# Optimization experiments

Hardware: AMD Instinct MI355X
Metric: run time of the kernel (lower is better)

## Reference

```python
import jax, jax.numpy as jnp
import numpy as np
from jax import lax

NPOINT = 1024
NSAMPLES = (16, 32, 64)
BN_EPS = 1e-5


def fps(xyz, npoint):
    """Farthest point sampling. xyz: [B,N,3] -> idx [B,npoint].
    Deterministic start at index 0 (torch version uses a random start)."""
    B, N, _ = xyz.shape

    def step(carry, _):
        dist, far = carry
        centroid = jnp.take_along_axis(xyz, far[:, None, None], axis=1)  # [B,1,3]
        d = jnp.sum((xyz - centroid) ** 2, axis=-1)                      # [B,N]
        dist = jnp.minimum(dist, d)
        nxt = jnp.argmax(dist, axis=1)
        return (dist, nxt), far

    init = (jnp.full((B, N), 1e10, xyz.dtype), jnp.zeros((B,), jnp.int32))
    _, idxs = lax.scan(step, init, None, length=npoint)  # [npoint,B]
    return idxs.T


def gather_points(points, idx):
    # points [B,N,C], idx [B,...] -> [B,...,C]
    return jax.vmap(lambda p, i: p[i])(points, idx)


def sq_cdist(a, b):
    # a [B,S,3], b [B,N,3] -> squared distances [B,S,N] (same ordering as cdist)
    aa = jnp.sum(a * a, -1)[:, :, None]
    bb = jnp.sum(b * b, -1)[:, None, :]
    return aa + bb - 2.0 * jnp.einsum('bsc,bnc->bsn', a, b)


def mlp_scale(g, ws, gs, bs):
    # g: [B,S,k,Cin]; 1x1 conv + BatchNorm (training-mode stats) + ReLU per layer
    for w, gm, bt in zip(ws, gs, bs):
        g = jnp.einsum('bskc,oc->bsko', g, w)
        mu = jnp.mean(g, axis=(0, 1, 2))
        var = jnp.var(g, axis=(0, 1, 2))
        g = jax.nn.relu((g - mu) * lax.rsqrt(var + BN_EPS) * gm + bt)
    return g


def setup_inputs() -> dict:
    key = jax.random.key(0)
    ks = jax.random.split(key, 16)
    B, N, C = 16, 4096, 64
    xyz = jax.random.normal(ks[0], (B, N, 3), jnp.float32)
    features = jax.random.normal(ks[1], (B, N, C), jnp.float32)
    # stacked per-scale MLP params; layer dims: 67 -> 64 -> 64 -> 128
    w0 = jax.random.normal(ks[2], (3, 64, 67), jnp.float32) * 0.1
    w1 = jax.random.normal(ks[3], (3, 64, 64), jnp.float32) * 0.1
    w2 = jax.random.normal(ks[4], (3, 128, 64), jnp.float32) * 0.1
    g0 = jnp.ones((3, 64), jnp.float32); b0 = jnp.zeros((3, 64), jnp.float32)
    g1 = jnp.ones((3, 64), jnp.float32); b1 = jnp.zeros((3, 64), jnp.float32)
    g2 = jnp.ones((3, 128), jnp.float32); b2 = jnp.zeros((3, 128), jnp.float32)
    return {"xyz": xyz, "features": features, "w0": w0, "w1": w1, "w2": w2,
            "g0": g0, "g1": g1, "g2": g2, "b0": b0, "b1": b1, "b2": b2}


def reference(xyz, features, w0, w1, w2, g0, g1, g2, b0, b1, b2):
    fps_idx = fps(xyz, NPOINT)                                   # [B,S]
    new_xyz = jnp.take_along_axis(xyz, fps_idx[..., None], axis=1)  # [B,S,3]
    d2 = sq_cdist(new_xyz, xyz)                                  # [B,S,N]
    outs = []
    for s, nsample in enumerate(NSAMPLES):
        _, idx = lax.top_k(-d2, nsample)                         # k nearest, [B,S,k]
        grouped_xyz = gather_points(xyz, idx) - new_xyz[:, :, None, :]
        grouped_f = gather_points(features, idx)
        g = jnp.concatenate([grouped_xyz, grouped_f], axis=-1)   # [B,S,k,67]
        g = mlp_scale(g, (w0[s], w1[s], w2[s]), (g0[s], g1[s], g2[s]), (b0[s], b1[s], b2[s]))
        outs.append(jnp.max(g, axis=2))                          # max over neighbors -> [B,S,128]
    fused = jnp.concatenate(outs, axis=-1)                       # [B,S,384]
    return new_xyz, fused
```

## Files before the change

### kernel.cpp

```cpp
#include <hip/hip_runtime.h>
#include <stdint.h>

#define BATCH 16
#define NPTS  4096
#define NSAMP 1024

typedef __attribute__((ext_vector_type(8))) short  short8;
typedef __attribute__((ext_vector_type(4))) float  floatx4;

__device__ __forceinline__ unsigned short f2bf(float f) {
    unsigned u = __float_as_uint(f);
    unsigned r = (u + 0x7FFFu + ((u >> 16) & 1u)) >> 16;
    return (unsigned short)r;
}

template<int CTRL>
__device__ __forceinline__ uint64_t dpp_max_u64(uint64_t k) {
    int lo = (int)(unsigned)k;
    int hi = (int)(unsigned)(k >> 32);
    int lo2 = __builtin_amdgcn_update_dpp(0, lo, CTRL, 0xF, 0xF, false);
    int hi2 = __builtin_amdgcn_update_dpp(0, hi, CTRL, 0xF, 0xF, false);
    uint64_t o = ((uint64_t)(unsigned)hi2 << 32) | (unsigned)lo2;
    return o > k ? o : k;
}

#define WT_S 18432

__global__ __launch_bounds__(512) void fps_conv_kernel(
    const float* __restrict__ xyz,
    float* __restrict__ out_xyz,
    const float* __restrict__ feat,
    unsigned short* __restrict__ featb,
    int staged,
    const float* __restrict__ w0, const float* __restrict__ w1,
    const float* __restrict__ w2, unsigned short* __restrict__ wtab)
{
#pragma clang fp contract(off)
    const int wbase = 16 + (staged ? 1024 : 0);
    if (blockIdx.x >= (unsigned)wbase) {
        int t = (blockIdx.x - wbase) * 512 + threadIdx.x;
        if (t < 3*WT_S) {
            int s = t / WT_S, r = t % WT_S;
            unsigned short v = 0;
            if (r < 6144) {
                int n = r / 96, kg = r % 96;
                if (kg < 67) {
                    int ci = (kg < 64) ? (kg + 3) : (kg - 64);
                    v = f2bf(w0[(size_t)(s*64 + n)*67 + ci]);
                }
            } else if (r < 10240) {
                int idx = r - 6144;
                v = f2bf(w1[(size_t)(s*64 + (idx >> 6))*64 + (idx & 63)]);
            } else {
                int idx = r - 10240;
                v = f2bf(w2[(size_t)(s*128 + (idx >> 6))*64 + (idx & 63)]);
            }
            wtab[t] = v;
        }
        return;
    }
    if (blockIdx.x >= 16) {
        int t = (blockIdx.x - 16) * 512 + threadIdx.x;
        const float4* fp = (const float4*)feat + (size_t)t*2;
        float4 a = fp[0], c = fp[1];
        uint4 o;
        o.x = (unsigned)f2bf(a.x) | ((unsigned)f2bf(a.y) << 16);
        o.y = (unsigned)f2bf(a.z) | ((unsigned)f2bf(a.w) << 16);
        o.z = (unsigned)f2bf(c.x) | ((unsigned)f2bf(c.y) << 16);
        o.w = (unsigned)f2bf(c.z) | ((unsigned)f2bf(c.w) << 16);
        ((uint4*)featb)[t] = o;
        return;
    }

    const int b    = blockIdx.x;
    const int tid  = threadIdx.x;
    const int lane = tid & 63;
    const int wave = tid >> 6;
    const float* xb = xyz + (size_t)b * NPTS * 3;

    __shared__ float xsh[NPTS], ysh[NPTS], zsh[NPTS];
    __shared__ float cents[NSAMP * 3];
    __shared__ uint64_t keylds[2][8];

    float px[8], py[8], pz[8], dist[8];
#pragma unroll
    for (int i = 0; i < 8; ++i) {
        int p = tid + (i << 9);
        px[i] = xb[p*3+0];
        py[i] = xb[p*3+1];
        pz[i] = xb[p*3+2];
        dist[i] = 1e10f;
        xsh[p] = px[i]; ysh[p] = py[i]; zsh[p] = pz[i];
    }
    __syncthreads();

    float cx = xb[0], cy = xb[1], cz = xb[2];

    for (int it = 0; it < NSAMP; ++it) {
        if (tid == 0) {
            cents[it*3+0] = cx; cents[it*3+1] = cy; cents[it*3+2] = cz;
        }
        if (it == NSAMP - 1) break;

#pragma unroll
        for (int i = 0; i < 8; ++i) {
            float dx = px[i] - cx, dy = py[i] - cy, dz = pz[i] - cz;
            float d = dx*dx; d = d + dy*dy; d = d + dz*dz;
            dist[i] = fminf(dist[i], d);
        }
        float w01 = dist[1] > dist[0] ? dist[1] : dist[0];
        int   e01 = dist[1] > dist[0] ? 1 : 0;
        float w23 = dist[3] > dist[2] ? dist[3] : dist[2];
        int   e23 = dist[3] > dist[2] ? 3 : 2;
        float w45 = dist[5] > dist[4] ? dist[5] : dist[4];
        int   e45 = dist[5] > dist[4] ? 5 : 4;
        float w67 = dist[7] > dist[6] ? dist[7] : dist[6];
        int   e67 = dist[7] > dist[6] ? 7 : 6;
        float wa  = w23 > w01 ? w23 : w01;
        int   ea  = w23 > w01 ? e23 : e01;
        float wb  = w67 > w45 ? w67 : w45;
        int   eb  = w67 > w45 ? e67 : e45;
        float wv  = wb > wa ? wb : wa;
        int   wi  = wb > wa ? eb : ea;
        unsigned widx = (unsigned)(tid + (wi << 9));
        uint64_t kk = ((uint64_t)__float_as_uint(wv) << 32) | (~widx);

        kk = dpp_max_u64<0x121>(kk);
        kk = dpp_max_u64<0x122>(kk);
        kk = dpp_max_u64<0x124>(kk);
        kk = dpp_max_u64<0x128>(kk);
        kk = dpp_max_u64<0x142>(kk);
        kk = dpp_max_u64<0x143>(kk);

        int pb = it & 1;
        if (lane == 63) keylds[pb][wave] = kk;
        __syncthreads();

        uint64_t f = keylds[pb][lane & 7];
        f = dpp_max_u64<0x121>(f);
        f = dpp_max_u64<0x122>(f);
        f = dpp_max_u64<0x124>(f);
        int cur = (int)~((unsigned)f);

        cx = xsh[cur]; cy = ysh[cur]; cz = zsh[cur];
    }

    __syncthreads();
    for (int i = tid; i < NSAMP*3; i += 512)
        out_xyz[(size_t)b*NSAMP*3 + i] = cents[i];
}

__global__ __launch_bounds__(1024) void knn_kernel(
    const float* __restrict__ xyz,
    const float* __restrict__ new_xyz,
    unsigned short* __restrict__ knn_idx)
{
#pragma clang fp contract(off)
    __shared__ float xs[NPTS], ys[NPTS], zs[NPTS];
    __shared__ uint64_t buf[16][64];
    const int tid  = threadIdx.x;
    const int lane = tid & 63;
    const int wave = tid >> 6;
    const int q = blockIdx.x * 16 + wave;
    const int b = q >> 10;
    const float* xb = xyz + (size_t)b * NPTS * 3;

    for (int i = tid; i < NPTS; i += 1024) {
        xs[i] = xb[i*3+0];
        ys[i] = xb[i*3+1];
        zs[i] = xb[i*3+2];
    }
    __syncthreads();

    const float qx = new_xyz[q*3+0], qy = new_xyz[q*3+1], qz = new_xyz[q*3+2];
    float aa = qx*qx; aa = aa + qy*qy; aa = aa + qz*qz;

    auto keyof = [&](int c) -> unsigned {
        float x = xs[c], y = ys[c], z = zs[c];
        float bb = x*x;  bb = bb + y*y;   bb = bb + z*z;
        float dt = qx*x; dt = dt + qy*y;  dt = dt + qz*z;
        float d2 = (aa + bb) - 2.0f*dt;
        unsigned u = __float_as_uint(d2);
        return (u & 0x80000000u) ? ~u : (u | 0x80000000u);
    };
    auto shfl64 = [&](uint64_t v, int src) -> uint64_t {
        int lo = __shfl((int)(unsigned)v, src);
        int hi = __shfl((int)(unsigned)(v >> 32), src);
        return ((uint64_t)(unsigned)hi << 32) | (unsigned)lo;
    };
    auto shflx64 = [&](uint64_t v, int m) -> uint64_t {
        int lo = __shfl_xor((int)(unsigned)v, m);
        int hi = __shfl_xor((int)(unsigned)(v >> 32), m);
        return ((uint64_t)(unsigned)hi << 32) | (unsigned)lo;
    };
    auto sortP = [&](uint64_t &p) {
#pragma unroll
        for (int kk = 2; kk <= 64; kk <<= 1) {
#pragma unroll
            for (int j = kk >> 1; j >= 1; j >>= 1) {
                uint64_t o = shflx64(p, j);
                bool up    = ((lane & kk) == 0);
                bool lower = ((lane & j) == 0);
                bool oless = o < p;
                bool keep  = (up == lower) ? oless : !oless;
                if (keep) p = o;
            }
        }
    };
    auto mergeP = [&](uint64_t &P, uint64_t Bv) {
        uint64_t rev = shfl64(Bv, 63 - lane);
        if (rev < P) P = rev;
#pragma unroll
        for (int j = 32; j >= 1; j >>= 1) {
            uint64_t o = shflx64(P, j);
            bool lower = ((lane & j) == 0);
            bool oless = o < P;
            bool keep  = lower ? oless : !oless;
            if (keep) P = o;
        }
    };

    uint64_t P = ((uint64_t)keyof(lane) << 32) | (unsigned)lane;
    sortP(P);
    uint64_t Pmax = shfl64(P, 63);
    int cnt = 0;

    for (int bt = 1; bt < 64; ++bt) {
        int c = (bt << 6) + lane;
        uint64_t cand = ((uint64_t)keyof(c) << 32) | (unsigned)c;
        bool qual = cand < Pmax;
        unsigned long long mask = __ballot(qual);
        if (mask == 0ull) continue;
        int n = __popcll(mask);
        if (cnt + n > 64) {
            uint64_t Bv = (lane < cnt) ? buf[wave][lane] : ~0ull;
            sortP(Bv);
            mergeP(P, Bv);
            Pmax = shfl64(P, 63);
            cnt = 0;
            qual = qual && (cand < Pmax);
            mask = __ballot(qual);
            n = __popcll(mask);
        }
        if (qual) {
            int pos = cnt + __popcll(mask & ((1ull << lane) - 1ull));
            buf[wave][pos] = cand;
        }
        cnt += n;
    }
    if (cnt > 0) {
        uint64_t Bv = (lane < cnt) ? buf[wave][lane] : ~0ull;
        sortP(Bv);
        mergeP(P, Bv);
    }
    knn_idx[(size_t)q*64 + lane] = (unsigned short)(P & 0xFFFFu);
}

#define GPB 8

template<int PHASE>
__global__ __launch_bounds__(256) void mlp_phase(
    const float* __restrict__ xyz,
    const float* __restrict__ feat,
    const float* __restrict__ new_xyz,
    const unsigned short* __restrict__ knn,
    const unsigned short* __restrict__ featb,
    int staged,
    const unsigned short* __restrict__ wtab,
    const float* __restrict__ bnp,
    float* __restrict__ stats,
    float* __restrict__ out1)
{
    __shared__ __align__(16) unsigned short g_lds[64*104];
    __shared__ __align__(16) unsigned short a_lds[64*72];
    __shared__ float stat_lds[256];
    __shared__ float wavemax[4*128];

    const int tid  = threadIdx.x;
    const int lane = tid & 63;
    const int wave = tid >> 6;
    const int n16  = lane & 15;
    const int quad = lane >> 4;

    int scale, g0;
    {
        int xcd = blockIdx.x & 7;
        int r   = blockIdx.x >> 3;
        int hi  = (r >= 224) ? 1 : 0;
        int bt  = 2*xcd + hi;
        int r2  = r - hi*224;
        if (r2 < 32)       { scale = 0; g0 = bt*256  + r2*GPB; }
        else if (r2 < 96)  { scale = 1; g0 = bt*512  + (r2-32)*GPB; }
        else               { scale = 2; g0 = bt*1024 + (r2-96)*GPB; }
    }
    const int KNB = 16 << scale;
    const int cpg = 4 >> scale;
    const int wpc = 1 << scale;

    const unsigned short* wt  = wtab + scale * WT_S;
    const unsigned short* w2b = wt + 6144;
    const unsigned short* w3b = wt + 10240;

    short8 w1f[4][3];
#pragma unroll
    for (int nt = 0; nt < 4; ++nt)
#pragma unroll
        for (int kb = 0; kb < 3; ++kb)
            w1f[nt][kb] = *(const short8*)&wt[(nt*16 + n16)*96 + kb*32 + quad*8];

    float s1p[4], t1p[4], s2p[4], t2p[4];
    if constexpr (PHASE >= 2) {
#pragma unroll
        for (int nt = 0; nt < 4; ++nt) {
            int o = ((0*3 + scale)*128 + nt*16 + n16)*2;
            s1p[nt] = bnp[o]; t1p[nt] = bnp[o+1];
        }
    }
    if constexpr (PHASE >= 3) {
#pragma unroll
        for (int nt = 0; nt < 4; ++nt) {
            int o = ((1*3 + scale)*128 + nt*16 + n16)*2;
            s2p[nt] = bnp[o]; t2p[nt] = bnp[o+1];
        }
    }

    float sac[8], sqac[8];
#pragma unroll
    for (int i = 0; i < 8; ++i) { sac[i] = 0.f; sqac[i] = 0.f; }
    stat_lds[tid] = 0.f;
    {
        const int r = tid >> 2;
        const int sub = tid & 3;
        if (sub == 0)      *(uint4*)&g_lds[r*104 + 72] = make_uint4(0u,0u,0u,0u);
        else if (sub == 1) *(uint4*)&g_lds[r*104 + 80] = make_uint4(0u,0u,0u,0u);
        else if (sub == 2) *(uint4*)&g_lds[r*104 + 88] = make_uint4(0u,0u,0u,0u);
    }
    __syncthreads();

    for (int g = g0; g < g0 + GPB; ++g) {
        const int cb = g * cpg;
        {
            const int r   = tid >> 2;
            const int sub = tid & 3;
            const int ci  = cb + (r >> (4 + scale));
            const int j   = r & (KNB - 1);
            const int n   = knn[(size_t)ci*64 + j];
            const int b   = ci >> 10;
            if (staged) {
                const unsigned short* frow = featb + ((size_t)(b*NPTS + n))*64 + sub*16;
                uint4 c0 = ((const uint4*)frow)[0];
                uint4 c1 = ((const uint4*)frow)[1];
                *(uint4*)&g_lds[r*104 + sub*16]     = c0;
                *(uint4*)&g_lds[r*104 + sub*16 + 8] = c1;
            } else {
                const float* frow = feat + ((size_t)(b*NPTS + n))*64 + sub*16;
                unsigned short h[16];
#pragma unroll
                for (int u = 0; u < 16; ++u) h[u] = f2bf(frow[u]);
                uint4 p0, p1;
                p0.x = (unsigned)h[0]  | ((unsigned)h[1]  << 16);
                p0.y = (unsigned)h[2]  | ((unsigned)h[3]  << 16);
                p0.z = (unsigned)h[4]  | ((unsigned)h[5]  << 16);
                p0.w = (unsigned)h[6]  | ((unsigned)h[7]  << 16);
                p1.x = (unsigned)h[8]  | ((unsigned)h[9]  << 16);
                p1.y = (unsigned)h[10] | ((unsigned)h[11] << 16);
                p1.z = (unsigned)h[12] | ((unsigned)h[13] << 16);
                p1.w = (unsigned)h[14] | ((unsigned)h[15] << 16);
                *(uint4*)&g_lds[r*104 + sub*16]     = p0;
                *(uint4*)&g_lds[r*104 + sub*16 + 8] = p1;
            }
            if (sub == 0) {
                const float* nx = new_xyz + (size_t)ci*3;
                const float* xp = xyz + ((size_t)(b*NPTS + n))*3;
                unsigned short h0 = f2bf(xp[0] - nx[0]);
                unsigned short h1 = f2bf(xp[1] - nx[1]);
                unsigned short h2 = f2bf(xp[2] - nx[2]);
                uint4 z = make_uint4((unsigned)h0 | ((unsigned)h1 << 16),
                                     (unsigned)h2, 0u, 0u);
                *(uint4*)&g_lds[r*104 + 64] = z;
            }
        }
        __syncthreads();

        const int rb = wave*16 + n16;
        short8 a0 = *(const short8*)&g_lds[rb*104 +      quad*8];
        short8 a1 = *(const short8*)&g_lds[rb*104 + 32 + quad*8];
        short8 a2 = *(const short8*)&g_lds[rb*104 + 64 + quad*8];
        floatx4 acc[4];
#pragma unroll
        for (int nt = 0; nt < 4; ++nt) {
            floatx4 c = {0.f,0.f,0.f,0.f};
            c = __builtin_amdgcn_mfma_f32_16x16x32_bf16(a0, w1f[nt][0], c, 0,0,0);
            c = __builtin_amdgcn_mfma_f32_16x16x32_bf16(a1, w1f[nt][1], c, 0,0,0);
            c = __builtin_amdgcn_mfma_f32_16x16x32_bf16(a2, w1f[nt][2], c, 0,0,0);
            acc[nt] = c;
        }

        if constexpr (PHASE == 1) {
#pragma unroll
            for (int nt = 0; nt < 4; ++nt) {
                floatx4 c = acc[nt];
                sac[nt]  += c[0]+c[1]+c[2]+c[3];
                sqac[nt] += c[0]*c[0]+c[1]*c[1]+c[2]*c[2]+c[3]*c[3];
            }
        }
        if constexpr (PHASE >= 2) {
#pragma unroll
            for (int nt = 0; nt < 4; ++nt) {
                int ch = nt*16 + n16;
#pragma unroll
                for (int r = 0; r < 4; ++r) {
                    float v = acc[nt][r]*s1p[nt] + t1p[nt];
                    v = fmaxf(v, 0.f);
                    a_lds[(wave*16 + quad*4 + r)*72 + ch] = f2bf(v);
                }
            }
            short8 e0 = *(const short8*)&a_lds[rb*72 +      quad*8];
            short8 e1 = *(const short8*)&a_lds[rb*72 + 32 + quad*8];
            floatx4 acc2[4];
#pragma unroll
            for (int nt = 0; nt < 4; ++nt) {
                short8 wa = *(const short8*)&w2b[(nt*16 + n16)*64 +      quad*8];
                short8 wb = *(const short8*)&w2b[(nt*16 + n16)*64 + 32 + quad*8];
                floatx4 c = {0.f,0.f,0.f,0.f};
                c = __builtin_amdgcn_mfma_f32_16x16x32_bf16(e0, wa, c, 0,0,0);
                c = __builtin_amdgcn_mfma_f32_16x16x32_bf16(e1, wb, c, 0,0,0);
                acc2[nt] = c;
            }
            if constexpr (PHASE == 2) {
#pragma unroll
                for (int nt = 0; nt < 4; ++nt) {
                    floatx4 c = acc2[nt];
                    sac[nt]  += c[0]+c[1]+c[2]+c[3];
                    sqac[nt] += c[0]*c[0]+c[1]*c[1]+c[2]*c[2]+c[3]*c[3];
                }
            }
            if constexpr (PHASE == 3) {
#pragma unroll
                for (int nt = 0; nt < 4; ++nt) {
                    int ch = nt*16 + n16;
#pragma unroll
                    for (int r = 0; r < 4; ++r) {
                        float v = acc2[nt][r]*s2p[nt] + t2p[nt];
                        v = fmaxf(v, 0.f);
                        a_lds[(wave*16 + quad*4 + r)*72 + ch] = f2bf(v);
                    }
                }
                short8 f0 = *(const short8*)&a_lds[rb*72 +      quad*8];
                short8 f1 = *(const short8*)&a_lds[rb*72 + 32 + quad*8];
#pragma unroll
                for (int nt = 0; nt < 8; ++nt) {
                    short8 wa = *(const short8*)&w3b[(nt*16 + n16)*64 +      quad*8];
                    short8 wb = *(const short8*)&w3b[(nt*16 + n16)*64 + 32 + quad*8];
                    floatx4 c = {0.f,0.f,0.f,0.f};
                    c = __builtin_amdgcn_mfma_f32_16x16x32_bf16(f0, wa, c, 0,0,0);
                    c = __builtin_amdgcn_mfma_f32_16x16x32_bf16(f1, wb, c, 0,0,0);
                    sac[nt]  += c[0]+c[1]+c[2]+c[3];
                    sqac[nt] += c[0]*c[0]+c[1]*c[1]+c[2]*c[2]+c[3]*c[3];
                    float m = fmaxf(fmaxf(c[0],c[1]), fmaxf(c[2],c[3]));
                    m = fmaxf(m, __shfl_xor(m, 16));
                    m = fmaxf(m, __shfl_xor(m, 32));
                    if (lane < 16) wavemax[wave*128 + nt*16 + n16] = m;
                }
            }
        }
        __syncthreads();
        if constexpr (PHASE == 3) {
            const int ch = tid & 127;
            for (int ic = tid >> 7; ic < cpg; ic += 2) {
                float m = wavemax[(ic*wpc)*128 + ch];
                for (int w = 1; w < wpc; ++w)
                    m = fmaxf(m, wavemax[(ic*wpc + w)*128 + ch]);
                out1[(size_t)(cb + ic)*384 + scale*128 + ch] = m;
            }
        }
    }

    const int NCH = (PHASE == 3) ? 8 : 4;
#pragma unroll
    for (int nt = 0; nt < 8; ++nt) {
        if (nt >= NCH) break;
        float v  = sac[nt], v2 = sqac[nt];
        v  += __shfl_xor(v, 16);  v  += __shfl_xor(v, 32);
        v2 += __shfl_xor(v2, 16); v2 += __shfl_xor(v2, 32);
        if (lane < 16) {
            int ch = nt*16 + n16;
            atomicAdd(&stat_lds[ch*2],   v);
            atomicAdd(&stat_lds[ch*2+1], v2);
        }
    }
    __syncthreads();
    const int layer = PHASE - 1;
    const int nch = (PHASE == 3) ? 128 : 64;
    if (tid < nch*2) {
        atomicAdd(&stats[(size_t)(layer*3 + scale)*256 + tid], stat_lds[tid]);
    }
}

__global__ void bn_params_kernel(
    const float* __restrict__ stats, float* __restrict__ bnp,
    const float* __restrict__ gamma, const float* __restrict__ beta,
    int layer, int nch)
{
    int t = blockIdx.x * blockDim.x + threadIdx.x;
    if (t >= 3*nch) return;
    int scale = t / nch, ch = t % nch;
    float M = 16384.0f * (float)(16 << scale);
    int o = ((layer*3 + scale)*128 + ch)*2;
    float sum = stats[o], sumsq = stats[o+1];
    float mean = sum / M;
    float var = sumsq / M - mean*mean;
    var = fmaxf(var, 0.f);
    float ga = gamma[scale*nch + ch];
    float be = beta[scale*nch + ch];
    float s  = ga / sqrtf(var + 1e-5f);
    float tt = be - mean * s;
    bnp[o] = s; bnp[o+1] = tt;
}

__global__ void finalize_kernel(
    const float* __restrict__ bnp,
    float* __restrict__ out1)
{
    int t = blockIdx.x * 256 + threadIdx.x;
    float4 m = ((const float4*)out1)[t];
    int c0 = (t*4) % 384;
    int scale = c0 >> 7;
    int ch = c0 & 127;
    int o = ((2*3 + scale)*128 + ch)*2;
    float4 r;
    r.x = fmaxf(m.x*bnp[o+0] + bnp[o+1], 0.f);
    r.y = fmaxf(m.y*bnp[o+2] + bnp[o+3], 0.f);
    r.z = fmaxf(m.z*bnp[o+4] + bnp[o+5], 0.f);
    r.w = fmaxf(m.w*bnp[o+6] + bnp[o+7], 0.f);
    ((float4*)out1)[t] = r;
}

extern "C" void kernel_launch(void* const* d_in, const int* in_sizes, int n_in,
                              void* d_out, int out_size, void* d_ws, size_t ws_size,
                              hipStream_t stream)
{
    (void)in_sizes; (void)n_in; (void)out_size;
    const float* xyz  = (const float*)d_in[0];
    const float* feat = (const float*)d_in[1];
    const float* w0   = (const float*)d_in[2];
    const float* w1   = (const float*)d_in[3];
    const float* w2   = (const float*)d_in[4];
    const float* g0   = (const float*)d_in[5];
    const float* g1   = (const float*)d_in[6];
    const float* g2   = (const float*)d_in[7];
    const float* b0   = (const float*)d_in[8];
    const float* b1   = (const float*)d_in[9];
    const float* b2   = (const float*)d_in[10];
    float* out  = (float*)d_out;
    float* out0 = out;
    float* out1 = out + 49152;

    char* ws = (char*)d_ws;
    const size_t NEED_FULL = 2097152ull + 8388608ull + 9216 + 9216 + 110592;
    const int staged = (ws_size >= NEED_FULL) ? 1 : 0;
    unsigned short* knn   = (unsigned short*)ws;
    unsigned short* featb = staged ? (unsigned short*)(ws + 2097152) : nullptr;
    size_t tail = staged ? (2097152ull + 8388608ull) : 2097152ull;
    float* stats = (float*)(ws + tail);
    float* bnp   = (float*)(ws + tail + 9216);
    unsigned short* wtab = (unsigned short*)(ws + tail + 18432);

    hipMemsetAsync(stats, 0, 9216, stream);
    fps_conv_kernel<<<16 + (staged ? 1024 : 0) + 108, 512, 0, stream>>>(
        xyz, out0, feat, featb, staged, w0, w1, w2, wtab);
    knn_kernel<<<1024, 1024, 0, stream>>>(xyz, out0, knn);

    mlp_phase<1><<<3584,256,0,stream>>>(xyz,feat,out0,knn,featb,staged,wtab,bnp,stats,out1);
    bn_params_kernel<<<1,256,0,stream>>>(stats, bnp, g0, b0, 0, 64);

    mlp_phase<2><<<3584,256,0,stream>>>(xyz,feat,out0,knn,featb,staged,wtab,bnp,stats,out1);
    bn_params_kernel<<<1,256,0,stream>>>(stats, bnp, g1, b1, 1, 64);

    mlp_phase<3><<<3584,256,0,stream>>>(xyz,feat,out0,knn,featb,staged,wtab,bnp,stats,out1);
    bn_params_kernel<<<2,256,0,stream>>>(stats, bnp, g2, b2, 2, 128);

    finalize_kernel<<<6144, 256, 0, stream>>>(bnp, out1);
}
```

Baseline: 1.298 ms.

## Prefetch next group's gathered features into registers during MFMA compute

Each iteration now issues the global gather (knn index, feature row and xyz offset) for the next group into registers before computing the current group. The registers are written to LDS after the compute barrier, followed by an extra barrier. This hides gather latency behind the MLP matrix work, at the cost of more live registers and one more sync per iteration.

After: 1.447 ms. 1.11x slower.

```diff
diff --git a/kernel.cpp b/kernel.cpp
--- a/kernel.cpp
+++ b/kernel.cpp
@@ -281,6 +281,8 @@
     const int wave = tid >> 6;
     const int n16  = lane & 15;
     const int quad = lane >> 4;
+    const int gr_r   = tid >> 2;
+    const int gr_sub = tid & 3;
 
     int scale, g0;
     {
@@ -329,58 +331,60 @@
     for (int i = 0; i < 8; ++i) { sac[i] = 0.f; sqac[i] = 0.f; }
     stat_lds[tid] = 0.f;
     {
-        const int r = tid >> 2;
-        const int sub = tid & 3;
-        if (sub == 0)      *(uint4*)&g_lds[r*104 + 72] = make_uint4(0u,0u,0u,0u);
-        else if (sub == 1) *(uint4*)&g_lds[r*104 + 80] = make_uint4(0u,0u,0u,0u);
-        else if (sub == 2) *(uint4*)&g_lds[r*104 + 88] = make_uint4(0u,0u,0u,0u);
-    }
+        if (gr_sub == 0)      *(uint4*)&g_lds[gr_r*104 + 72] = make_uint4(0u,0u,0u,0u);
+        else if (gr_sub == 1) *(uint4*)&g_lds[gr_r*104 + 80] = make_uint4(0u,0u,0u,0u);
+        else if (gr_sub == 2) *(uint4*)&g_lds[gr_r*104 + 88] = make_uint4(0u,0u,0u,0u);
+    }
+
+    auto stage_load = [&](int gq, uint4& c0, uint4& c1, uint4& z) {
+        const int cb2 = gq * cpg;
+        const int ci  = cb2 + (gr_r >> (4 + scale));
+        const int j   = gr_r & (KNB - 1);
+        const int n   = knn[(size_t)ci*64 + j];
+        const int b   = ci >> 10;
+        if (staged) {
+            const unsigned short* frow = featb + ((size_t)(b*NPTS + n))*64 + gr_sub*16;
+            c0 = ((const uint4*)frow)[0];
+            c1 = ((const uint4*)frow)[1];
+        } else {
+            const float* frow = feat + ((size_t)(b*NPTS + n))*64 + gr_sub*16;
+            unsigned short h[16];
+#pragma unroll
+            for (int u = 0; u < 16; ++u) h[u] = f2bf(frow[u]);
+            c0.x = (unsigned)h[0]  | ((unsigned)h[1]  << 16);
+            c0.y = (unsigned)h[2]  | ((unsigned)h[3]  << 16);
+            c0.z = (unsigned)h[4]  | ((unsigned)h[5]  << 16);
+            c0.w = (unsigned)h[6]  | ((unsigned)h[7]  << 16);
+            c1.x = (unsigned)h[8]  | ((unsigned)h[9]  << 16);
+            c1.y = (unsigned)h[10] | ((unsigned)h[11] << 16);
+            c1.z = (unsigned)h[12] | ((unsigned)h[13] << 16);
+            c1.w = (unsigned)h[14] | ((unsigned)h[15] << 16);
+        }
+        if (gr_sub == 0) {
+            const float* nx = new_xyz + (size_t)ci*3;
+            const float* xp = xyz + ((size_t)(b*NPTS + n))*3;
+            unsigned short h0 = f2bf(xp[0] - nx[0]);
+            unsigned short h1 = f2bf(xp[1] - nx[1]);
+            unsigned short h2 = f2bf(xp[2] - nx[2]);
+            z = make_uint4((unsigned)h0 | ((unsigned)h1 << 16),
+                           (unsigned)h2, 0u, 0u);
+        }
+    };
+    auto stage_write = [&](const uint4& c0, const uint4& c1, const uint4& z) {
+        *(uint4*)&g_lds[gr_r*104 + gr_sub*16]     = c0;
+        *(uint4*)&g_lds[gr_r*104 + gr_sub*16 + 8] = c1;
+        if (gr_sub == 0) *(uint4*)&g_lds[gr_r*104 + 64] = z;
+    };
+
+    uint4 sc0, sc1, sz;
+    stage_load(g0, sc0, sc1, sz);
+    stage_write(sc0, sc1, sz);
     __syncthreads();
 
     for (int g = g0; g < g0 + GPB; ++g) {
-        const int cb = g * cpg;
-        {
-            const int r   = tid >> 2;
-            const int sub = tid & 3;
-            const int ci  = cb + (r >> (4 + scale));
-            const int j   = r & (KNB - 1);
-            const int n   = knn[(size_t)ci*64 + j];
-            const int b   = ci >> 10;
-            if (staged) {
-                const unsigned short* frow = featb + ((size_t)(b*NPTS + n))*64 + sub*16;
-                uint4 c0 = ((const uint4*)frow)[0];
-                uint4 c1 = ((const uint4*)frow)[1];
-                *(uint4*)&g_lds[r*104 + sub*16]     = c0;
-                *(uint4*)&g_lds[r*104 + sub*16 + 8] = c1;
-            } else {
-                const float* frow = feat + ((size_t)(b*NPTS + n))*64 + sub*16;
-                unsigned short h[16];
-#pragma unroll
-                for (int u = 0; u < 16; ++u) h[u] = f2bf(frow[u]);
-                uint4 p0, p1;
-                p0.x = (unsigned)h[0]  | ((unsigned)h[1]  << 16);
-                p0.y = (unsigned)h[2]  | ((unsigned)h[3]  << 16);
-                p0.z = (unsigned)h[4]  | ((unsigned)h[5]  << 16);
-                p0.w = (unsigned)h[6]  | ((unsigned)h[7]  << 16);
-                p1.x = (unsigned)h[8]  | ((unsigned)h[9]  << 16);
-                p1.y = (unsigned)h[10] | ((unsigned)h[11] << 16);
-                p1.z = (unsigned)h[12] | ((unsigned)h[13] << 16);
-                p1.w = (unsigned)h[14] | ((unsigned)h[15] << 16);
-                *(uint4*)&g_lds[r*104 + sub*16]     = p0;
-                *(uint4*)&g_lds[r*104 + sub*16 + 8] = p1;
-            }
-            if (sub == 0) {
-                const float* nx = new_xyz + (size_t)ci*3;
-                const float* xp = xyz + ((size_t)(b*NPTS + n))*3;
-                unsigned short h0 = f2bf(xp[0] - nx[0]);
-                unsigned short h1 = f2bf(xp[1] - nx[1]);
-                unsigned short h2 = f2bf(xp[2] - nx[2]);
-                uint4 z = make_uint4((unsigned)h0 | ((unsigned)h1 << 16),
-                                     (unsigned)h2, 0u, 0u);
-                *(uint4*)&g_lds[r*104 + 64] = z;
-            }
-        }
-        __syncthreads();
+        const int cb   = g * cpg;
+        const bool more = (g + 1 < g0 + GPB);
+        if (more) stage_load(g + 1, sc0, sc1, sz);
 
         const int rb = wave*16 + n16;
         short8 a0 = *(const short8*)&g_lds[rb*104 +      quad*8];
@@ -465,6 +469,8 @@
             }
         }
         __syncthreads();
+
+        if (more) stage_write(sc0, sc1, sz);
         if constexpr (PHASE == 3) {
             const int ch = tid & 127;
             for (int ic = tid >> 7; ic < cpg; ic += 2) {
@@ -474,6 +480,7 @@
                 out1[(size_t)(cb + ic)*384 + scale*128 + ch] = m;
             }
         }
+        __syncthreads();
     }
 
     const int NCH = (PHASE == 3) ? 8 : 4;
```
